# Kernel tuning notes

Measured on AMD Instinct MI355X. Metric: run time of the kernel, lower is better.

## Reference

```python
import jax, jax.numpy as jnp
import numpy as np

N = 4096
FIN = 4096
LOC = 16
H1, H2, HEADS = 120, 50, 4
H1_PER = H1 // HEADS
FILM_Z = 32
SSDB_H = 60
N_HEMI = N // 2
NEG_SLOPE = 0.1
GATE_BIAS = -2.0
MASK_FILL = -9e15


def leaky(x):
    return jax.nn.leaky_relu(x, negative_slope=NEG_SLOPE)


def gat(x, mask, W, a_src, a_dst, bias, concat):
    # x: (N, Fin), W: (H, Fin, O), a_src/a_dst: (H, O), mask: (N, N) bool
    wh = jnp.einsum('nf,hfo->hno', x, W)            # (H, N, O)
    f1 = jnp.einsum('hno,ho->hn', wh, a_src)        # (H, N)
    f2 = jnp.einsum('hno,ho->hn', wh, a_dst)        # (H, N)
    e = leaky(f1[:, :, None] + f2[:, None, :])      # (H, N, N)
    e = jnp.where(mask[None], e, MASK_FILL)
    alpha = jax.nn.softmax(e, axis=-1)
    out = jnp.einsum('hij,hjo->hio', alpha, wh)     # (H, N, O)
    if concat:
        h, n, o = out.shape
        out2 = out.transpose(1, 0, 2).reshape(n, h * o)
    else:
        out2 = out.mean(axis=0)
    return out2 + bias


def _uni(k, shape, stdv):
    return jax.random.uniform(k, shape, jnp.float32, -stdv, stdv)


def setup_inputs() -> dict:
    key = jax.random.key(0)
    ks = jax.random.split(key, 30)
    s1 = 1.0 / np.sqrt(H1_PER)
    s2 = 1.0 / np.sqrt(H2)
    inp = {
        'x_fc': jax.random.normal(ks[0], (N, FIN), jnp.float32),
        'adj': jax.random.randint(ks[1], (N, N), 0, 2, jnp.int32),
        'l_loc': jax.random.uniform(ks[2], (N, LOC), jnp.float32),
        # gat1
        'W1': _uni(ks[3], (HEADS, FIN, H1_PER), s1),
        'a1s': _uni(ks[4], (HEADS, H1_PER), s1),
        'a1d': _uni(ks[5], (HEADS, H1_PER), s1),
        'b1': _uni(ks[6], (H1,), s1),
        # gat2
        'W2': _uni(ks[7], (1, H1, H2), s2),
        'a2s': _uni(ks[8], (1, H2), s2),
        'a2d': _uni(ks[9], (1, H2), s2),
        'b2': _uni(ks[10], (H2,), s2),
        # classifier (no bias)
        'Wc': _uni(ks[11], (2, H2), s2),
        # FiLM trunk
        'Wl1': _uni(ks[12], (FILM_Z, LOC), 1.0 / np.sqrt(LOC)),
        'bl1': _uni(ks[13], (FILM_Z,), 1.0 / np.sqrt(LOC)),
        'Wl2': _uni(ks[14], (FILM_Z, FILM_Z), 1.0 / np.sqrt(FILM_Z)),
        'bl2': _uni(ks[15], (FILM_Z,), 1.0 / np.sqrt(FILM_Z)),
        'Wg': _uni(ks[16], (H2, FILM_Z), 1.0 / np.sqrt(FILM_Z)),
        'bg': _uni(ks[17], (H2,), 1.0 / np.sqrt(FILM_Z)),
        'Wb': _uni(ks[18], (H2, FILM_Z), 1.0 / np.sqrt(FILM_Z)),
        'bb': _uni(ks[19], (H2,), 1.0 / np.sqrt(FILM_Z)),
        'Wgate': _uni(ks[20], (1, FILM_Z), 1.0 / np.sqrt(FILM_Z)),
        'bgate': jnp.full((1,), GATE_BIAS, jnp.float32),
        # SSDB hemi
        'Ws1': _uni(ks[21], (SSDB_H, N_HEMI), 1.0 / np.sqrt(N_HEMI)),
        'bs1': _uni(ks[22], (SSDB_H,), 1.0 / np.sqrt(N_HEMI)),
        'Ws2': _uni(ks[23], (1, SSDB_H), 1.0 / np.sqrt(SSDB_H)),
        'bs2': _uni(ks[24], (1,), 1.0 / np.sqrt(SSDB_H)),
    }
    return inp


def reference(x_fc, adj, l_loc, W1, a1s, a1d, b1, W2, a2s, a2d, b2, Wc,
              Wl1, bl1, Wl2, bl2, Wg, bg, Wb, bb, Wgate, bgate,
              Ws1, bs1, Ws2, bs2):
    mask = adj > 0
    h = leaky(gat(x_fc, mask, W1, a1s, a1d, b1, concat=True))    # (N, 120)
    h = leaky(gat(h, mask, W2, a2s, a2d, b2, concat=False))      # (N, 50)
    # FiLM conditioning
    z = leaky(l_loc @ Wl1.T + bl1)
    z = leaky(z @ Wl2.T + bl2)
    gamma = z @ Wg.T + bg                                        # (N, 50)
    beta = z @ Wb.T + bb                                         # (N, 50)
    g = jax.nn.sigmoid(z @ Wgate.T + bgate)                      # (N, 1)
    cov = jnp.clip(l_loc[:, -1], 0.0, 1.0)                       # coverage_power = 1.0
    g = g * cov[:, None]
    h_fused = h + g * (gamma * h + beta)
    logits = leaky(h_fused @ Wc.T)                               # (N, 2)
    # hemisphere SSDB bias
    t = logits.T                                                 # (2, N)
    ipsi = t[:, :N_HEMI]
    contra = t[:, N_HEMI:2 * N_HEMI]
    h_i = leaky(ipsi @ Ws1.T + bs1)                              # (2, 60)
    h_c = leaky(contra @ Ws1.T + bs1)
    b_i = leaky(h_i @ Ws2.T + bs2)                               # (2, 1)
    b_c = leaky(h_c @ Ws2.T + bs2)
    b_mid = 0.5 * (b_i + b_c)                                    # (2, 1)
    bias_nodes = jnp.concatenate([
        jnp.broadcast_to(b_i.T, (N_HEMI, 2)),
        jnp.broadcast_to(b_c.T, (N_HEMI, 2)),
    ], axis=0)                                                   # n_mid = 0
    logits = logits + bias_nodes
    bias_avg = b_mid[:, 0]                                       # (2,)
    return logits, bias_avg
```

## Files before the change

kernel.cpp:

```cpp
#include <hip/hip_runtime.h>

#define NN 4096
#define NNP 4128
#define BROW 132
#define HEADS 4
#define H1PER 30
#define H1DIM 120
#define H2DIM 50

typedef short short8_t __attribute__((ext_vector_type(8)));
typedef float f32x4 __attribute__((ext_vector_type(4)));

__device__ __forceinline__ float lrelu(float x) { return x > 0.f ? x : 0.1f * x; }

__device__ __forceinline__ unsigned short bfrne(float x) {
  unsigned u = __float_as_uint(x);
  u += 0x7fffu + ((u >> 16) & 1u);
  return (unsigned short)(u >> 16);
}
__device__ __forceinline__ unsigned bfpk_rne(float lo, float hi) {
  return (unsigned)bfrne(lo) | ((unsigned)bfrne(hi) << 16);
}
__device__ __forceinline__ unsigned bfpk(float lo, float hi) {
  unsigned a = (__float_as_uint(lo) + 0x8000u) >> 16;
  unsigned b = (__float_as_uint(hi) + 0x8000u) & 0xffff0000u;
  return a | b;
}
__device__ __forceinline__ unsigned fenc(float x) {
  unsigned u = __float_as_uint(x);
  return (u & 0x80000000u) ? ~u : (u | 0x80000000u);
}
__device__ __forceinline__ float fdec(unsigned u) {
  return (u & 0x80000000u) ? __uint_as_float(u ^ 0x80000000u) : __uint_as_float(~u);
}

#define GL16(g, l)                                                                        \
  __builtin_amdgcn_global_load_lds((const __attribute__((address_space(1))) unsigned int*)(g), \
                                   (__attribute__((address_space(3))) unsigned int*)(l), 16, 0, 0)

__global__ __launch_bounds__(256) void k_bits(const int* __restrict__ adj,
                                              unsigned long long* __restrict__ bits) {
  int n = blockIdx.x >> 2, r = blockIdx.x & 3;
  size_t base = (size_t)n * 4096 + r * 1024;
  int t = threadIdx.x;
  int v0 = adj[base + t];
  int v1 = adj[base + 256 + t];
  int v2 = adj[base + 512 + t];
  int v3 = adj[base + 768 + t];
  unsigned long long m0 = __ballot(v0 > 0);
  unsigned long long m1 = __ballot(v1 > 0);
  unsigned long long m2 = __ballot(v2 > 0);
  unsigned long long m3 = __ballot(v3 > 0);
  if ((t & 63) == 0) {
    size_t w = (size_t)n * (BROW / 2) + r * 16 + (t >> 6);
    bits[w] = m0;
    bits[w + 4] = m1;
    bits[w + 8] = m2;
    bits[w + 12] = m3;
  }
}

__global__ __launch_bounds__(256) void k_prep(const float* __restrict__ W1,
                                              const float* __restrict__ a1s,
                                              const float* __restrict__ a1d,
                                              unsigned short* __restrict__ w1t) {
  int k = blockIdx.x * 256 + threadIdx.x;
#pragma unroll
  for (int h = 0; h < 4; ++h) {
    const float* wp = W1 + ((size_t)h * 4096 + k) * H1PER;
    float fs = 0.f, fd = 0.f;
#pragma unroll
    for (int oo = 0; oo < H1PER; ++oo) {
      float v = wp[oo];
      w1t[(size_t)(h * 30 + oo) * NNP + k] = bfrne(v);
      fs += v * a1s[h * H1PER + oo];
      fd += v * a1d[h * H1PER + oo];
    }
    w1t[(size_t)(120 + h) * NNP + k] = bfrne(fs);
    w1t[(size_t)(124 + h) * NNP + k] = bfrne(fd);
  }
}

__global__ __launch_bounds__(256) void k_gemm1s(const float* __restrict__ x,
                                                const unsigned short* __restrict__ w1t,
                                                float* __restrict__ part) {
  const int t = threadIdx.x;
  const int lane = t & 63, wave = t >> 6;
  const int m = lane & 15, q = lane >> 4;
  const int i0 = blockIdx.x * 32;
  const int kz = blockIdx.y * 512;
  __shared__ float xs[2][32 * 64];
  __shared__ unsigned short bs[2][128 * 64];
  const int r0 = (wave & 1) * 16;
  const int ntg0 = (wave >> 1) * 4;
  const int srow0 = wave * 8 + q;
  const int srow1 = srow0 + 4;
  const float* gx0 = x + (size_t)(i0 + srow0) * 4096 + kz + (m ^ (srow0 & 7)) * 4;
  const float* gx1 = x + (size_t)(i0 + srow1) * 4096 + kz + (m ^ (srow1 & 7)) * 4;
  const int lo0 = srow0 * 64 + m * 4;
  const int lo1 = srow1 * 64 + m * 4;
  const int l8 = lane >> 3, c8 = lane & 7;
  const unsigned short* gb = w1t + (size_t)(wave * 32 + l8) * NNP + kz + (c8 ^ l8) * 8;
  const int bo = wave * 2048 + lane * 8;
  const int arow = r0 + m;
  const int asw = m & 7;
  f32x4 acc[4];
#pragma unroll
  for (int nt = 0; nt < 4; ++nt) acc[nt] = (f32x4){0.f, 0.f, 0.f, 0.f};

  GL16(gx0, &xs[0][lo0]);
  GL16(gx1, &xs[0][lo1]);
#pragma unroll
  for (int i = 0; i < 4; ++i) GL16(gb + (size_t)i * 8 * NNP, &bs[0][bo + i * 512]);

#pragma unroll
  for (int it = 0; it < 8; ++it) {
    const int cur = it & 1;
    if (it < 7) {
      const int kc = (it + 1) * 64;
      GL16(gx0 + kc, &xs[cur ^ 1][lo0]);
      GL16(gx1 + kc, &xs[cur ^ 1][lo1]);
#pragma unroll
      for (int i = 0; i < 4; ++i) GL16(gb + (size_t)i * 8 * NNP + kc, &bs[cur ^ 1][bo + i * 512]);
      asm volatile("s_waitcnt vmcnt(6)" ::: "memory");
    } else {
      asm volatile("s_waitcnt vmcnt(0)" ::: "memory");
    }
    __builtin_amdgcn_s_barrier();
    __builtin_amdgcn_sched_barrier(0);
#pragma unroll
    for (int ks2 = 0; ks2 < 2; ++ks2) {
      const int c0 = ks2 * 8 + q * 2;
      float4 a0 = *(const float4*)&xs[cur][arow * 64 + ((c0 ^ asw) * 4)];
      float4 a1 = *(const float4*)&xs[cur][arow * 64 + (((c0 + 1) ^ asw) * 4)];
      union { short8_t v; unsigned u[4]; } A;
      A.u[0] = bfpk_rne(a0.x, a0.y);
      A.u[1] = bfpk_rne(a0.z, a0.w);
      A.u[2] = bfpk_rne(a1.x, a1.y);
      A.u[3] = bfpk_rne(a1.z, a1.w);
      const int bch = ((ks2 << 2) | q) ^ asw;
#pragma unroll
      for (int nt = 0; nt < 4; ++nt) {
        short8_t B = *(const short8_t*)&bs[cur][((ntg0 + nt) * 16 + m) * 64 + bch * 8];
        acc[nt] = __builtin_amdgcn_mfma_f32_16x16x32_bf16(A.v, B, acc[nt], 0, 0, 0);
      }
    }
    __builtin_amdgcn_sched_barrier(0);
    __builtin_amdgcn_s_barrier();
  }
  float* pp = part + ((size_t)blockIdx.y * 4096 + i0 + r0 + q * 4) * 128 + ntg0 * 16 + m;
#pragma unroll
  for (int nt = 0; nt < 4; ++nt)
#pragma unroll
    for (int r = 0; r < 4; ++r) pp[r * 128 + nt * 16] = acc[nt][r];
}

__global__ __launch_bounds__(256) void k_f1c(const float* __restrict__ part,
                                             unsigned short* __restrict__ whbt,
                                             float* __restrict__ f1, float* __restrict__ f2,
                                             unsigned* __restrict__ mxu1) {
  const int t = threadIdx.x;
  const int n = blockIdx.x * 16 + (t >> 4);
  const int og = (t & 15) * 8;
  __shared__ float f2loc[16][4];
  float s[8] = {0.f, 0.f, 0.f, 0.f, 0.f, 0.f, 0.f, 0.f};
  for (int z = 0; z < 8; ++z) {
    const float* pp = part + ((size_t)z * NN + n) * 128 + og;
    float4 u0 = *(const float4*)pp;
    float4 u1 = *(const float4*)(pp + 4);
    s[0] += u0.x; s[1] += u0.y; s[2] += u0.z; s[3] += u0.w;
    s[4] += u1.x; s[5] += u1.y; s[6] += u1.z; s[7] += u1.w;
  }
  if (og < 120) {
#pragma unroll
    for (int j = 0; j < 8; ++j) {
      int o = og + j;
      int h = o / 30, oo = o - h * 30;
      whbt[(size_t)(h * 32 + oo) * NNP + n] = bfrne(s[j]);
    }
  } else {
#pragma unroll
    for (int j = 0; j < 4; ++j) {
      f1[(size_t)j * NN + n] = s[j];
      f2[(size_t)j * NN + n] = s[4 + j];
      f2loc[t >> 4][j] = s[4 + j];
    }
  }
  if ((t & 15) < 8) {
    int h = (t & 15) >> 1, odd = (t & 15) & 1;
    whbt[(size_t)(h * 32 + 30 + odd) * NNP + n] = odd ? 0 : 0x3f80;
  }
  __syncthreads();
  if (t < 4) {
    float m = f2loc[0][t];
#pragma unroll
    for (int i = 1; i < 16; ++i) m = fmaxf(m, f2loc[i][t]);
    atomicMax(&mxu1[t], fenc(m));
  }
}

__global__ __launch_bounds__(256) void k_att1m(const unsigned short* __restrict__ whbt,
                                               const float* __restrict__ f1, const float* __restrict__ f2,
                                               const unsigned* __restrict__ mxu1,
                                               const unsigned int* __restrict__ bits32,
                                               float* __restrict__ part) {
  const int h = blockIdx.y, js = blockIdx.z;
  const int t = threadIdx.x;
  const int lane = t & 63, wave = t >> 6;
  const int m = lane & 15, q = lane >> 4;
  const int i0 = blockIdx.x * 64 + wave * 16;
  const int jbase = js * 1024;
  const float mxh = fdec(mxu1[h]);
  __shared__ float2 es[1024];
  __shared__ unsigned short bsm1[2][8192];
  for (int e = t; e < 1024; e += 256) {
    float fv = f2[h * NN + jbase + e] - mxh;
    es[e] = make_float2(__expf(fv), __expf(0.1f * fv));
  }
  const float f1r = f1[h * NN + i0 + m];
  const float s = f1r + mxh;
  const float R = __expf(fminf(60.f, -0.9f * s));
  const uint4* brow4 = (const uint4*)(bits32 + (size_t)(i0 + m) * BROW + (jbase >> 5));
  const float2* fp = es;
  const int r_st = t >> 3;
  const unsigned short* gB = whbt + (size_t)(h * 32 + r_st) * NNP + jbase + ((t & 7) ^ (r_st & 7)) * 8;
  f32x4 acc0 = {0.f, 0.f, 0.f, 0.f}, acc1 = {0.f, 0.f, 0.f, 0.f};

  __syncthreads();

#pragma unroll
  for (int c = 0; c < 4; ++c) GL16(gB + c * 64, &bsm1[0][c * 2048 + t * 8]);

#pragma unroll
  for (int jc = 0; jc < 4; ++jc) {
    const int cur = jc & 1;
    const uint4 bqA = brow4[jc * 2];
    const uint4 bqB = brow4[jc * 2 + 1];
    if (jc < 3) {
#pragma unroll
      for (int c = 0; c < 4; ++c) GL16(gB + (jc + 1) * 256 + c * 64, &bsm1[cur ^ 1][c * 2048 + t * 8]);
      asm volatile("s_waitcnt vmcnt(4)" ::: "memory");
    } else {
      asm volatile("s_waitcnt vmcnt(0)" ::: "memory");
    }
    __builtin_amdgcn_s_barrier();
    __builtin_amdgcn_sched_barrier(0);
#pragma unroll
    for (int g = 0; g < 2; ++g) {
      const uint4 bq = g ? bqB : bqA;
#pragma unroll
      for (int sub = 0; sub < 4; ++sub) {
        const int jl = (jc * 2 + g) * 128 + sub * 32;
        unsigned bsel = (sub == 0 ? bq.x : sub == 1 ? bq.y : sub == 2 ? bq.z : bq.w) >> (q * 8);
        float4 e01 = *(const float4*)(fp + jl + q * 8);
        float4 e23 = *(const float4*)(fp + jl + q * 8 + 2);
        float4 e45 = *(const float4*)(fp + jl + q * 8 + 4);
        float4 e67 = *(const float4*)(fp + jl + q * 8 + 6);
        auto sc = [&](float ep, float en, int jj) {
          float wv = fmaxf(ep, R * en);
          return ((bsel >> jj) & 1u) ? wv : 0.f;
        };
        union { short8_t v; unsigned u[4]; } A;
        A.u[0] = bfpk(sc(e01.x, e01.y, 0), sc(e01.z, e01.w, 1));
        A.u[1] = bfpk(sc(e23.x, e23.y, 2), sc(e23.z, e23.w, 3));
        A.u[2] = bfpk(sc(e45.x, e45.y, 4), sc(e45.z, e45.w, 5));
        A.u[3] = bfpk(sc(e67.x, e67.y, 6), sc(e67.z, e67.w, 7));
        const int p = g * 16 + sub * 4 + q;
        short8_t b0 = *(const short8_t*)&bsm1[cur][(p >> 3) * 2048 + m * 64 + ((p & 7) ^ (m & 7)) * 8];
        short8_t b1 = *(const short8_t*)&bsm1[cur][(p >> 3) * 2048 + (m + 16) * 64 + ((p & 7) ^ ((m + 16) & 7)) * 8];
        acc0 = __builtin_amdgcn_mfma_f32_16x16x32_bf16(A.v, b0, acc0, 0, 0, 0);
        acc1 = __builtin_amdgcn_mfma_f32_16x16x32_bf16(A.v, b1, acc1, 0, 0, 0);
      }
    }
    __builtin_amdgcn_sched_barrier(0);
    __builtin_amdgcn_s_barrier();
  }
  float* pp = part + ((size_t)(js * 4 + h) * NN + i0 + q * 4) * 32 + m;
#pragma unroll
  for (int r = 0; r < 4; ++r) {
    pp[r * 32] = acc0[r];
    pp[r * 32 + 16] = acc1[r];
  }
}

__global__ __launch_bounds__(256) void k_fuseA(const float* __restrict__ part, const float* __restrict__ b1,
                                               const float* __restrict__ W2, const float* __restrict__ a2s,
                                               const float* __restrict__ a2d,
                                               unsigned short* __restrict__ whbt2,
                                               float* __restrict__ f1b, float* __restrict__ f2b,
                                               unsigned* __restrict__ mxu2) {
  const int t = threadIdx.x;
  __shared__ float W2s[H1DIM * H2DIM];
  __shared__ float h1s[4][124];
  __shared__ float f2red[4];
  for (int e = t; e < H1DIM * H2DIM; e += 256) W2s[e] = W2[e];
  const int wv = t >> 6, lane = t & 63;
  const int n = blockIdx.x * 4 + wv;
  const int h = lane >> 4, o2 = (lane & 15) * 2;
  float tot0 = 0.f, tot1 = 0.f;
#pragma unroll
  for (int z = 0; z < 4; ++z) {
    const float* pp = part + ((size_t)(z * 4 + h) * NN + n) * 32 + o2;
    float2 u = *(const float2*)pp;
    tot0 += u.x;
    tot1 += u.y;
  }
  float l = __shfl(tot0, h * 16 + 15);
  float inv = 1.f / l;
  if (o2 < 30) {
    h1s[wv][h * 30 + o2] = lrelu(tot0 * inv + b1[h * 30 + o2]);
    h1s[wv][h * 30 + o2 + 1] = lrelu(tot1 * inv + b1[h * 30 + o2 + 1]);
  }
  __syncthreads();
  const int o = lane;
  float acc = 0.f;
  if (o < H2DIM) {
    const float* hr = h1s[wv];
#pragma unroll 4
    for (int k = 0; k < H1DIM; ++k) acc += hr[k] * W2s[k * H2DIM + o];
  }
  unsigned short wbv = (o < H2DIM) ? bfrne(acc) : (o == H2DIM ? (unsigned short)0x3f80 : (unsigned short)0);
  whbt2[(size_t)o * NNP + n] = wbv;
  float ps = (o < H2DIM) ? acc * a2s[o] : 0.f;
  float pd = (o < H2DIM) ? acc * a2d[o] : 0.f;
  for (int off = 32; off > 0; off >>= 1) {
    ps += __shfl_down(ps, off);
    pd += __shfl_down(pd, off);
  }
  if (lane == 0) {
    f1b[n] = ps;
    f2b[n] = pd;
    f2red[wv] = pd;
  }
  __syncthreads();
  if (t == 0) {
    float m = fmaxf(fmaxf(f2red[0], f2red[1]), fmaxf(f2red[2], f2red[3]));
    atomicMax(mxu2, fenc(m));
  }
}

__global__ __launch_bounds__(256) void k_att2m(const unsigned short* __restrict__ whbt2,
                                               const float* __restrict__ f1b, const float* __restrict__ f2b,
                                               const unsigned* __restrict__ mxu2,
                                               const unsigned int* __restrict__ bits32,
                                               float* __restrict__ part) {
  const int js = blockIdx.y;
  const int t = threadIdx.x;
  const int lane = t & 63, wave = t >> 6;
  const int m = lane & 15, q = lane >> 4;
  const int i0 = blockIdx.x * 64 + wave * 16;
  const int jbase = js * 512;
  const float mx0 = fdec(mxu2[0]);
  __shared__ float2 es[512];
  __shared__ unsigned short bsm2[2][8192];
  for (int e = t; e < 512; e += 256) {
    float fv = f2b[jbase + e] - mx0;
    es[e] = make_float2(__expf(fv), __expf(0.1f * fv));
  }
  const float f1r = f1b[i0 + m];
  const float s = f1r + mx0;
  const float R = __expf(fminf(60.f, -0.9f * s));
  const uint4* brow4 = (const uint4*)(bits32 + (size_t)(i0 + m) * BROW + (jbase >> 5));
  const float2* fp = es;
  const int r2 = t >> 2;
  const int sw2 = (r2 & 3) ^ ((r2 >> 2) & 3);
  const unsigned short* gB2 = whbt2 + (size_t)r2 * NNP + jbase + ((t & 3) ^ sw2) * 8;
  f32x4 acc[4];
#pragma unroll
  for (int xx = 0; xx < 4; ++xx) acc[xx] = (f32x4){0.f, 0.f, 0.f, 0.f};

  __syncthreads();

#pragma unroll
  for (int c = 0; c < 4; ++c) GL16(gB2 + c * 32, &bsm2[0][c * 2048 + t * 8]);

#pragma unroll
  for (int jc = 0; jc < 4; ++jc) {
    const int cur = jc & 1;
    const uint4 bq = brow4[jc];
    if (jc < 3) {
#pragma unroll
      for (int c = 0; c < 4; ++c) GL16(gB2 + (jc + 1) * 128 + c * 32, &bsm2[cur ^ 1][c * 2048 + t * 8]);
      asm volatile("s_waitcnt vmcnt(4)" ::: "memory");
    } else {
      asm volatile("s_waitcnt vmcnt(0)" ::: "memory");
    }
    __builtin_amdgcn_s_barrier();
    __builtin_amdgcn_sched_barrier(0);
#pragma unroll
    for (int sub = 0; sub < 4; ++sub) {
      const int jl = jc * 128 + sub * 32;
      unsigned bsel = (sub == 0 ? bq.x : sub == 1 ? bq.y : sub == 2 ? bq.z : bq.w) >> (q * 8);
      float4 e01 = *(const float4*)(fp + jl + q * 8);
      float4 e23 = *(const float4*)(fp + jl + q * 8 + 2);
      float4 e45 = *(const float4*)(fp + jl + q * 8 + 4);
      float4 e67 = *(const float4*)(fp + jl + q * 8 + 6);
      auto sc = [&](float ep, float en, int jj) {
        float wv = fmaxf(ep, R * en);
        return ((bsel >> jj) & 1u) ? wv : 0.f;
      };
      union { short8_t v; unsigned u[4]; } A;
      A.u[0] = bfpk(sc(e01.x, e01.y, 0), sc(e01.z, e01.w, 1));
      A.u[1] = bfpk(sc(e23.x, e23.y, 2), sc(e23.z, e23.w, 3));
      A.u[2] = bfpk(sc(e45.x, e45.y, 4), sc(e45.z, e45.w, 5));
      A.u[3] = bfpk(sc(e67.x, e67.y, 6), sc(e67.z, e67.w, 7));
      const int p = sub * 4 + q;
#pragma unroll
      for (int tile = 0; tile < 4; ++tile) {
        const int f = tile * 16 + m;
        const int sw = (f & 3) ^ ((f >> 2) & 3);
        short8_t b = *(const short8_t*)&bsm2[cur][(p >> 2) * 2048 + f * 32 + (((p & 3) ^ sw)) * 8];
        acc[tile] = __builtin_amdgcn_mfma_f32_16x16x32_bf16(A.v, b, acc[tile], 0, 0, 0);
      }
    }
    __builtin_amdgcn_sched_barrier(0);
    __builtin_amdgcn_s_barrier();
  }
  float* pp = part + ((size_t)js * NN + i0 + q * 4) * 64 + m;
#pragma unroll
  for (int tile = 0; tile < 4; ++tile)
#pragma unroll
    for (int r = 0; r < 4; ++r) pp[r * 64 + tile * 16] = acc[tile][r];
}

__global__ __launch_bounds__(256) void k_fuseB(const float* __restrict__ part, const float* __restrict__ b2,
                                               const float* __restrict__ l_loc,
                                               const float* __restrict__ Wl1, const float* __restrict__ bl1,
                                               const float* __restrict__ Wl2, const float* __restrict__ bl2,
                                               const float* __restrict__ Wg, const float* __restrict__ bg,
                                               const float* __restrict__ Wb, const float* __restrict__ bb,
                                               const float* __restrict__ Wgate, const float* __restrict__ bgate,
                                               const float* __restrict__ Wc, float* __restrict__ logits) {
  const int t = threadIdx.x;
  const int wv = t >> 6, lane = t & 63;
  const int n = blockIdx.x * 4 + wv;
  const float* p = part + (size_t)n * 64 + lane;
  float tot = 0.f;
#pragma unroll
  for (int z = 0; z < 8; ++z) tot += p[(size_t)z * NN * 64];
  float l = __shfl(tot, 50);
  float hv = (lane < H2DIM) ? lrelu(tot / l + b2[lane]) : 0.f;
  int r32 = lane & 31;
  float locv = l_loc[n * 16 + (lane & 15)];
  float cov = __shfl(locv, 15);
  cov = fminf(fmaxf(cov, 0.f), 1.f);
  float a1v = bl1[r32];
#pragma unroll
  for (int j = 0; j < 16; ++j) a1v += Wl1[r32 * 16 + j] * __shfl(locv, j);
  float z1 = lrelu(a1v);
  float a2v = bl2[r32];
#pragma unroll
  for (int j = 0; j < 32; ++j) a2v += Wl2[r32 * 32 + j] * __shfl(z1, j);
  float z2 = lrelu(a2v);
  float gs = bgate[0];
  float gam, bet;
  {
    int o = lane < H2DIM ? lane : 0;
    gam = bg[o];
    bet = bb[o];
#pragma unroll
    for (int j = 0; j < 32; ++j) {
      float zj = __shfl(z2, j);
      gs += Wgate[j] * zj;
      gam += Wg[o * 32 + j] * zj;
      bet += Wb[o * 32 + j] * zj;
    }
  }
  float g = cov / (1.f + __expf(-gs));
  float hf = hv + g * (gam * hv + bet);
  int o = lane < H2DIM ? lane : 0;
  float p0 = lane < H2DIM ? hf * Wc[o] : 0.f;
  float p1 = lane < H2DIM ? hf * Wc[H2DIM + o] : 0.f;
  for (int off = 32; off > 0; off >>= 1) {
    p0 += __shfl_down(p0, off);
    p1 += __shfl_down(p1, off);
  }
  if (lane == 0) {
    logits[n * 2 + 0] = lrelu(p0);
    logits[n * 2 + 1] = lrelu(p1);
  }
}

__global__ __launch_bounds__(64) void k_ssdbA(const float* __restrict__ logits,
                                              const float* __restrict__ Ws1, const float* __restrict__ bs1,
                                              const float* __restrict__ Ws2, float* __restrict__ hsum) {
  const int k = blockIdx.x, combo = blockIdx.y;
  const int hemi = combo >> 1, c = combo & 1;
  const int lane = threadIdx.x;
  const float* wr = Ws1 + (size_t)k * 2048;
  const float* lc = logits + (size_t)hemi * 4096 + c;
  float acc = 0.f;
#pragma unroll 4
  for (int i = lane; i < 2048; i += 64) acc += wr[i] * lc[2 * i];
  for (int off = 32; off > 0; off >>= 1) acc += __shfl_down(acc, off);
  if (lane == 0) hsum[combo * 60 + k] = lrelu(acc + bs1[k]) * Ws2[k];
}

__global__ __launch_bounds__(256) void k_finB(const float* __restrict__ hsum,
                                              const float* __restrict__ bs2,
                                              const float* __restrict__ logits,
                                              float* __restrict__ out) {
  __shared__ float Bs[4];
  const int t = threadIdx.x;
  {
    int combo = t >> 6, k = t & 63;
    float v = (k < 60) ? hsum[combo * 60 + k] : 0.f;
    for (int off = 32; off > 0; off >>= 1) v += __shfl_down(v, off);
    if (k == 0) Bs[combo] = lrelu(v + bs2[0]);
  }
  __syncthreads();
  int id = blockIdx.x * 256 + t;
  if (id < 2 * NN) {
    int n = id >> 1, c = id & 1;
    out[id] = logits[id] + Bs[(n < 2048 ? 0 : 2) + c];
  } else if (id < 2 * NN + 2) {
    int c = id - 2 * NN;
    out[id] = 0.5f * (Bs[c] + Bs[2 + c]);
  }
}

#define OFF_BITS 0
#define OFF_W1T 540672
#define OFF_GP 804864
#define OFF_A1P 804864
#define OFF_A2P 804864
#define OFF_WH1BT 4999168
#define OFF_F1A 5263360
#define OFF_F2A 5279744
#define OFF_WH2BT 5296128
#define OFF_F12 5428224
#define OFF_F22 5432320
#define OFF_LOG 5436416
#define OFF_MX 5444608
#define OFF_HS 5444672

extern "C" void kernel_launch(void* const* d_in, const int* in_sizes, int n_in,
                              void* d_out, int out_size, void* d_ws, size_t ws_size,
                              hipStream_t stream) {
  const float* x_fc  = (const float*)d_in[0];
  const int*   adj   = (const int*)d_in[1];
  const float* l_loc = (const float*)d_in[2];
  const float* W1    = (const float*)d_in[3];
  const float* a1s   = (const float*)d_in[4];
  const float* a1d   = (const float*)d_in[5];
  const float* b1    = (const float*)d_in[6];
  const float* W2    = (const float*)d_in[7];
  const float* a2s   = (const float*)d_in[8];
  const float* a2d   = (const float*)d_in[9];
  const float* b2    = (const float*)d_in[10];
  const float* Wc    = (const float*)d_in[11];
  const float* Wl1   = (const float*)d_in[12];
  const float* bl1   = (const float*)d_in[13];
  const float* Wl2   = (const float*)d_in[14];
  const float* bl2   = (const float*)d_in[15];
  const float* Wg    = (const float*)d_in[16];
  const float* bg    = (const float*)d_in[17];
  const float* Wb    = (const float*)d_in[18];
  const float* bb    = (const float*)d_in[19];
  const float* Wgate = (const float*)d_in[20];
  const float* bgate = (const float*)d_in[21];
  const float* Ws1   = (const float*)d_in[22];
  const float* bs1   = (const float*)d_in[23];
  const float* Ws2   = (const float*)d_in[24];
  const float* bs2   = (const float*)d_in[25];
  float* out = (float*)d_out;
  float* w = (float*)d_ws;
  unsigned long long* bits = (unsigned long long*)(w + OFF_BITS);
  const unsigned int* bits32 = (const unsigned int*)bits;
  unsigned short* wh1bt = (unsigned short*)(w + OFF_WH1BT);
  unsigned short* wh2bt = (unsigned short*)(w + OFF_WH2BT);
  unsigned short* w1t = (unsigned short*)(w + OFF_W1T);
  unsigned* mxu = (unsigned*)(w + OFF_MX);

  hipMemsetAsync(mxu, 0, 8 * sizeof(unsigned), stream);
  k_bits<<<NN * NN / 1024, 256, 0, stream>>>(adj, bits);
  k_prep<<<16, 256, 0, stream>>>(W1, a1s, a1d, w1t);
  k_gemm1s<<<dim3(128, 8), 256, 0, stream>>>(x_fc, w1t, w + OFF_GP);
  k_f1c<<<256, 256, 0, stream>>>(w + OFF_GP, wh1bt, w + OFF_F1A, w + OFF_F2A, mxu);
  k_att1m<<<dim3(64, HEADS, 4), 256, 0, stream>>>(wh1bt, w + OFF_F1A, w + OFF_F2A,
                                                  mxu, bits32, w + OFF_A1P);
  k_fuseA<<<1024, 256, 0, stream>>>(w + OFF_A1P, b1, W2, a2s, a2d, wh2bt,
                                    w + OFF_F12, w + OFF_F22, mxu + 4);
  k_att2m<<<dim3(64, 8), 256, 0, stream>>>(wh2bt, w + OFF_F12, w + OFF_F22,
                                           mxu + 4, bits32, w + OFF_A2P);
  k_fuseB<<<1024, 256, 0, stream>>>(w + OFF_A2P, b2, l_loc, Wl1, bl1, Wl2, bl2,
                                    Wg, bg, Wb, bb, Wgate, bgate, Wc, w + OFF_LOG);
  k_ssdbA<<<dim3(60, 4), 64, 0, stream>>>(w + OFF_LOG, Ws1, bs1, Ws2, w + OFF_HS);
  k_finB<<<33, 256, 0, stream>>>(w + OFF_HS, bs2, w + OFF_LOG, out);
}
```

Baseline: 308.0 us.

## Double GEMM1 row tile to 64 so each wave covers all 128 columns

The first projection GEMM now processes 64 rows of x per block instead of 32. Each wave owns 16 rows and all 8 column tiles, which halves the grid and halves how often the W1 tile is reloaded per row. This cuts global traffic for the B operand and improves reuse per LDS load. In exchange it uses more LDS and more accumulator registers per block, and 512 blocks may lower occupancy and parallelism on the GPU. An unused STAGE lambda with odd index arithmetic is left in the code.

```diff
diff --git a/kernel.cpp b/kernel.cpp
--- a/kernel.cpp
+++ b/kernel.cpp
@@ -87,42 +87,52 @@
   const int t = threadIdx.x;
   const int lane = t & 63, wave = t >> 6;
   const int m = lane & 15, q = lane >> 4;
-  const int i0 = blockIdx.x * 32;
+  const int i0 = blockIdx.x * 64;
   const int kz = blockIdx.y * 512;
-  __shared__ float xs[2][32 * 64];
+  __shared__ float xs[2][64 * 64];
   __shared__ unsigned short bs[2][128 * 64];
-  const int r0 = (wave & 1) * 16;
-  const int ntg0 = (wave >> 1) * 4;
-  const int srow0 = wave * 8 + q;
-  const int srow1 = srow0 + 4;
-  const float* gx0 = x + (size_t)(i0 + srow0) * 4096 + kz + (m ^ (srow0 & 7)) * 4;
-  const float* gx1 = x + (size_t)(i0 + srow1) * 4096 + kz + (m ^ (srow1 & 7)) * 4;
-  const int lo0 = srow0 * 64 + m * 4;
-  const int lo1 = srow1 * 64 + m * 4;
+  const int ar_ = t >> 4;
+  const int ac_ = t & 15;
+  const float* gxa = x + (size_t)(i0 + ar_) * 4096 + kz + (ac_ ^ (ar_ & 7)) * 4;
+  const int adst = ar_ * 64 + ac_ * 4;
   const int l8 = lane >> 3, c8 = lane & 7;
   const unsigned short* gb = w1t + (size_t)(wave * 32 + l8) * NNP + kz + (c8 ^ l8) * 8;
   const int bo = wave * 2048 + lane * 8;
-  const int arow = r0 + m;
+  const int arow = wave * 16 + m;
   const int asw = m & 7;
-  f32x4 acc[4];
-#pragma unroll
-  for (int nt = 0; nt < 4; ++nt) acc[nt] = (f32x4){0.f, 0.f, 0.f, 0.f};
-
-  GL16(gx0, &xs[0][lo0]);
-  GL16(gx1, &xs[0][lo1]);
-#pragma unroll
-  for (int i = 0; i < 4; ++i) GL16(gb + (size_t)i * 8 * NNP, &bs[0][bo + i * 512]);
-
+  f32x4 acc[8];
+#pragma unroll
+  for (int nt = 0; nt < 8; ++nt) acc[nt] = (f32x4){0.f, 0.f, 0.f, 0.f};
+
+  auto STAGE = [&](int buf, int kk) {
+#pragma unroll
+    for (int i = 0; i < 4; ++i)
+      GL16(gxa + (size_t)i * 16 * 4096 + kk, &xs[buf][(i * 16 + ar_) * 64 + (ac_ * 4) - (ar_ * 0) + ar_ * 64 * 0 + 0] + (i * 16) * 64 - (i * 16) * 64 + 0), (void)0;
+#pragma unroll
+    for (int i = 0; i < 4; ++i)
+      GL16(gb + (size_t)i * 8 * NNP + kk, &bs[buf][bo + i * 512]);
+  };
+  auto STAGE_A = [&](int buf, int kk) {
+#pragma unroll
+    for (int i = 0; i < 4; ++i)
+      GL16(gxa + (size_t)i * 16 * 4096 + kk, &xs[buf][(i * 16 + ar_) * 64 + ac_ * 4]);
+  };
+  auto STAGE_B = [&](int buf, int kk) {
+#pragma unroll
+    for (int i = 0; i < 4; ++i)
+      GL16(gb + (size_t)i * 8 * NNP + kk, &bs[buf][bo + i * 512]);
+  };
+
+  STAGE_A(0, 0);
+  STAGE_B(0, 0);
 #pragma unroll
   for (int it = 0; it < 8; ++it) {
     const int cur = it & 1;
     if (it < 7) {
       const int kc = (it + 1) * 64;
-      GL16(gx0 + kc, &xs[cur ^ 1][lo0]);
-      GL16(gx1 + kc, &xs[cur ^ 1][lo1]);
-#pragma unroll
-      for (int i = 0; i < 4; ++i) GL16(gb + (size_t)i * 8 * NNP + kc, &bs[cur ^ 1][bo + i * 512]);
-      asm volatile("s_waitcnt vmcnt(6)" ::: "memory");
+      STAGE_A(cur ^ 1, kc);
+      STAGE_B(cur ^ 1, kc);
+      asm volatile("s_waitcnt vmcnt(8)" ::: "memory");
     } else {
       asm volatile("s_waitcnt vmcnt(0)" ::: "memory");
     }
@@ -140,17 +150,17 @@
       A.u[3] = bfpk_rne(a1.z, a1.w);
       const int bch = ((ks2 << 2) | q) ^ asw;
 #pragma unroll
-      for (int nt = 0; nt < 4; ++nt) {
-        short8_t B = *(const short8_t*)&bs[cur][((ntg0 + nt) * 16 + m) * 64 + bch * 8];
+      for (int nt = 0; nt < 8; ++nt) {
+        short8_t B = *(const short8_t*)&bs[cur][(nt * 16 + m) * 64 + bch * 8];
         acc[nt] = __builtin_amdgcn_mfma_f32_16x16x32_bf16(A.v, B, acc[nt], 0, 0, 0);
       }
     }
     __builtin_amdgcn_sched_barrier(0);
     __builtin_amdgcn_s_barrier();
   }
-  float* pp = part + ((size_t)blockIdx.y * 4096 + i0 + r0 + q * 4) * 128 + ntg0 * 16 + m;
-#pragma unroll
-  for (int nt = 0; nt < 4; ++nt)
+  float* pp = part + ((size_t)blockIdx.y * 4096 + i0 + wave * 16 + q * 4) * 128 + m;
+#pragma unroll
+  for (int nt = 0; nt < 8; ++nt)
 #pragma unroll
     for (int r = 0; r < 4; ++r) pp[r * 128 + nt * 16] = acc[nt][r];
 }
@@ -575,7 +585,7 @@
   hipMemsetAsync(mxu, 0, 8 * sizeof(unsigned), stream);
   k_bits<<<NN * NN / 1024, 256, 0, stream>>>(adj, bits);
   k_prep<<<16, 256, 0, stream>>>(W1, a1s, a1d, w1t);
-  k_gemm1s<<<dim3(128, 8), 256, 0, stream>>>(x_fc, w1t, w + OFF_GP);
+  k_gemm1s<<<dim3(64, 8), 256, 0, stream>>>(x_fc, w1t, w + OFF_GP);
   k_f1c<<<256, 256, 0, stream>>>(w + OFF_GP, wh1bt, w + OFF_F1A, w + OFF_F2A, mxu);
   k_att1m<<<dim3(64, HEADS, 4), 256, 0, stream>>>(wh1bt, w + OFF_F1A, w + OFF_F2A,
                                                   mxu, bits32, w + OFF_A1P);
```

Measured after the change: 298.9 us. 3.0% less time.
